# Kernel optimization log

Hardware: AMD Instinct MI355X
Metric: run time of the kernel (lower is better)

## Reference

```python
import jax, jax.numpy as jnp
import numpy as np

DIM = 1024
HEADS = 16
HEAD_DIM = DIM // HEADS
EPS = 1e-5


def setup_inputs() -> dict:
    key = jax.random.key(0)
    ks = jax.random.split(key, 4)
    N, L = 4, 2048
    x = jax.random.normal(ks[0], (N, L, DIM), dtype=jnp.float32)
    # causal mask: True means masked (strictly upper triangle)
    attn_mask = jnp.triu(jnp.ones((L, L), dtype=jnp.bool_), k=1)[None, None, :, :]
    w_qkv = jax.random.normal(ks[1], (3 * DIM, DIM), dtype=jnp.float32) * (DIM ** -0.5)
    w_proj = jax.random.normal(ks[2], (DIM, DIM), dtype=jnp.float32) * (DIM ** -0.5)
    b_proj = jnp.zeros((DIM,), dtype=jnp.float32)
    q_gamma = jnp.ones((HEAD_DIM,), dtype=jnp.float32)
    q_beta = jnp.zeros((HEAD_DIM,), dtype=jnp.float32)
    k_gamma = jnp.ones((HEAD_DIM,), dtype=jnp.float32)
    k_beta = jnp.zeros((HEAD_DIM,), dtype=jnp.float32)
    return {"x": x, "attn_mask": attn_mask, "w_qkv": w_qkv, "w_proj": w_proj,
            "b_proj": b_proj, "q_gamma": q_gamma, "q_beta": q_beta,
            "k_gamma": k_gamma, "k_beta": k_beta}


def _layernorm(h, gamma, beta):
    mu = jnp.mean(h, axis=-1, keepdims=True)
    var = jnp.mean(jnp.square(h - mu), axis=-1, keepdims=True)
    return (h - mu) * jax.lax.rsqrt(var + EPS) * gamma + beta


def reference(x, attn_mask, w_qkv, w_proj, b_proj, q_gamma, q_beta, k_gamma, k_beta):
    N, L, D = x.shape
    H, hd = HEADS, HEAD_DIM
    scale = hd ** -0.5
    qkv = jnp.einsum('nld,ed->nle', x, w_qkv)  # [N, L, 3D]
    qkv = qkv.reshape(N, L, 3, H, hd).transpose(2, 0, 3, 1, 4)  # [3, N, H, L, hd]
    q, k, v = qkv[0], qkv[1], qkv[2]
    q = _layernorm(q, q_gamma, q_beta)
    k = _layernorm(k, k_gamma, k_beta)
    scores = jnp.einsum('nhqd,nhkd->nhqk', q * scale, k)
    scores = scores + jnp.where(attn_mask, -jnp.inf, 0.0).astype(scores.dtype)
    attn = jax.nn.softmax(scores, axis=-1)
    out = jnp.einsum('nhqk,nhkd->nhqd', attn, v)  # [N, H, L, hd]
    out = out.transpose(0, 2, 1, 3).reshape(N, L, D)
    return jnp.einsum('nld,ed->nle', out, w_proj) + b_proj
```

## Files before the change

kernel.cpp:

```cpp
#include <hip/hip_runtime.h>


using f16x8 = __attribute__((ext_vector_type(8))) _Float16;
using f16x4 = __attribute__((ext_vector_type(4))) _Float16;
using f16x2 = __attribute__((ext_vector_type(2))) _Float16;
using f32x4 = __attribute__((ext_vector_type(4))) float;
using f32x16 = __attribute__((ext_vector_type(16))) float;
using u32x4 = __attribute__((ext_vector_type(4))) unsigned int;

#define MFMA16(a, b, c) __builtin_amdgcn_mfma_f32_16x16x32_f16(a, b, c, 0, 0, 0)
#define MFMA32(a, b, c) __builtin_amdgcn_mfma_f32_32x32x16_f16(a, b, c, 0, 0, 0)

__device__ __forceinline__ void gload_lds16(const void* g, void* l) {
  __builtin_amdgcn_global_load_lds(
      (const __attribute__((address_space(1))) unsigned int*)g,
      (__attribute__((address_space(3))) unsigned int*)l, 16, 0, 0);
}

__device__ __forceinline__ float dot2acc(unsigned int pk, float c) {
#if __has_builtin(__builtin_amdgcn_fdot2)
  const f16x2 ones = {(_Float16)1.f, (_Float16)1.f};
  return __builtin_amdgcn_fdot2(__builtin_bit_cast(f16x2, pk), ones, c, false);
#else
  f16x2 v = __builtin_bit_cast(f16x2, pk);
  return c + (float)v[0] + (float)v[1];
#endif
}

__global__ __launch_bounds__(256) void f32_to_f16_kernel(
    const float* __restrict__ in, _Float16* __restrict__ out, int n) {
  int i = (blockIdx.x * 256 + threadIdx.x) * 8;
  if (i >= n) return;
  float4 a = *(const float4*)(in + i);
  float4 b = *(const float4*)(in + i + 4);
  f16x8 o;
  o[0] = (_Float16)a.x; o[1] = (_Float16)a.y; o[2] = (_Float16)a.z; o[3] = (_Float16)a.w;
  o[4] = (_Float16)b.x; o[5] = (_Float16)b.y; o[6] = (_Float16)b.z; o[7] = (_Float16)b.w;
  *(f16x8*)(out + i) = o;
}

template <int MODE>
__global__ __launch_bounds__(256, 2) void gemm_bt(
    const _Float16* __restrict__ A, const _Float16* __restrict__ B,
    void* __restrict__ Cout, const float* __restrict__ bias,
    const float* __restrict__ qg, const float* __restrict__ qb,
    const float* __restrict__ kg, const float* __restrict__ kb,
    int M, int N, int K) {
  __shared__ __align__(16) _Float16 As[3][128 * 32];
  __shared__ __align__(16) _Float16 Bs[3][256 * 32];
  const int tid = threadIdx.x;
  const int w = tid >> 6, lane = tid & 63;
  const int c = lane & 15, g = lane >> 4;
  const long mbase = (long)blockIdx.x * 128;
  const long nbase = (long)blockIdx.y * 256;
  const int wm = (w >> 1) * 64, wn = (w & 1) * 128;
  const int sr4 = lane >> 2;
  const int scol = ((lane & 3) ^ ((lane >> 3) & 3)) * 8;
  const int sg = (g ^ ((c >> 1) & 3)) * 8;
  const char* pAr = (const char*)As + (wm + c) * 64 + sg * 2;
  const char* pBr = (const char*)Bs + (wn + c) * 64 + sg * 2;

#define GSTAGE(aOff_, bOff_, kt_)                                             \
  {                                                                           \
    const int kk_ = (kt_) * 32;                                               \
    _Pragma("unroll") for (int i = 0; i < 2; ++i) {                           \
      const int arow = w * 32 + i * 16 + sr4;                                 \
      gload_lds16(A + (mbase + arow) * K + kk_ + scol,                        \
                  (char*)As + (aOff_) + (w * 2 + i) * 1024);                  \
    }                                                                         \
    _Pragma("unroll") for (int j = 0; j < 4; ++j) {                           \
      const int brow = w * 64 + j * 16 + sr4;                                 \
      gload_lds16(B + (nbase + brow) * K + kk_ + scol,                        \
                  (char*)Bs + (bOff_) + (w * 4 + j) * 1024);                  \
    }                                                                         \
  }

  f32x4 acc[4][8];
#pragma unroll
  for (int i = 0; i < 4; ++i)
#pragma unroll
    for (int j = 0; j < 8; ++j) acc[i][j] = f32x4{0.f, 0.f, 0.f, 0.f};

  const int nk = K >> 5;
  GSTAGE(0, 0, 0);
  GSTAGE(8192, 16384, 1);
  int aR = 0, bR = 0;
  int aS = 16384, bS = 32768;
  for (int kt = 0; kt < nk; ++kt) {
    if (kt + 1 < nk) {
      asm volatile("s_waitcnt vmcnt(6)" ::: "memory");
    } else {
      asm volatile("s_waitcnt vmcnt(0)" ::: "memory");
    }
    __builtin_amdgcn_sched_barrier(0);
    __builtin_amdgcn_s_barrier();
    __builtin_amdgcn_sched_barrier(0);
    f16x8 af[4], bfr[8];
#pragma unroll
    for (int mt = 0; mt < 4; ++mt)
      af[mt] = *(const f16x8*)(pAr + aR + mt * 1024);
#pragma unroll
    for (int nt = 0; nt < 8; ++nt)
      bfr[nt] = *(const f16x8*)(pBr + bR + nt * 1024);
    if (kt + 2 < nk) GSTAGE(aS, bS, kt + 2);
    __builtin_amdgcn_s_setprio(1);
#pragma unroll
    for (int mt = 0; mt < 4; ++mt)
#pragma unroll
      for (int nt = 0; nt < 8; ++nt)
        acc[mt][nt] = MFMA16(af[mt], bfr[nt], acc[mt][nt]);
    __builtin_amdgcn_s_setprio(0);
    aR = (aR == 16384) ? 0 : aR + 8192;
    bR = (bR == 32768) ? 0 : bR + 16384;
    aS = (aS == 16384) ? 0 : aS + 8192;
    bS = (bS == 32768) ? 0 : bS + 16384;
  }
#undef GSTAGE

  if constexpr (MODE == 1) {
    const int region = (int)(nbase >> 10);
    if (region < 2) {
      const float* gamma = region ? kg : qg;
      const float* beta = region ? kb : qb;
      float gam[4], bet[4];
#pragma unroll
      for (int j = 0; j < 4; ++j) {
        gam[j] = gamma[j * 16 + c];
        bet[j] = beta[j * 16 + c];
      }
      const float sc = region ? 1.f : 0.1803368801111204f;
#pragma unroll
      for (int mt = 0; mt < 4; ++mt)
#pragma unroll
        for (int hh = 0; hh < 2; ++hh)
#pragma unroll
          for (int r = 0; r < 4; ++r) {
            float s1 = 0.f, s2 = 0.f;
#pragma unroll
            for (int j = 0; j < 4; ++j) {
              const float v = acc[mt][hh * 4 + j][r];
              s1 += v;
              s2 += v * v;
            }
#pragma unroll
            for (int msk = 1; msk < 16; msk <<= 1) {
              s1 += __shfl_xor(s1, msk);
              s2 += __shfl_xor(s2, msk);
            }
            const float mu = s1 * 0.015625f;
            const float rstd = rsqrtf(s2 * 0.015625f - mu * mu + 1e-5f);
#pragma unroll
            for (int j = 0; j < 4; ++j)
              acc[mt][hh * 4 + j][r] =
                  ((acc[mt][hh * 4 + j][r] - mu) * rstd * gam[j] + bet[j]) * sc;
          }
    }
#pragma unroll
    for (int nt = 0; nt < 8; ++nt) {
      const long col = nbase + wn + nt * 16 + c;
#pragma unroll
      for (int mt = 0; mt < 4; ++mt)
#pragma unroll
        for (int r = 0; r < 4; ++r) {
          const long row = mbase + wm + mt * 16 + g * 4 + r;
          ((_Float16*)Cout)[row * N + col] = (_Float16)acc[mt][nt][r];
        }
    }
  } else {
#pragma unroll
    for (int nt = 0; nt < 8; ++nt) {
      const long col = nbase + wn + nt * 16 + c;
      const float bv = bias ? bias[col] : 0.f;
#pragma unroll
      for (int mt = 0; mt < 4; ++mt)
#pragma unroll
        for (int r = 0; r < 4; ++r) {
          const long row = mbase + wm + mt * 16 + g * 4 + r;
          ((float*)Cout)[row * N + col] = acc[mt][nt][r] + bv;
        }
    }
  }
}

__global__ __launch_bounds__(256) void transpose_v_kernel(
    const _Float16* __restrict__ qkv, _Float16* __restrict__ Vt) {
  __shared__ __align__(16) _Float16 tile[64][80];
  const int nh = blockIdx.y;
  const long n = nh >> 4;
  const int h = nh & 15;
  const long lbase = (long)blockIdx.x * 64;
  const int t = threadIdx.x;
#pragma unroll
  for (int r = 0; r < 2; ++r) {
    const int l = (t + r * 256) >> 3;
    const int cc = (t & 7) * 8;
    f16x8 v = *(const f16x8*)(qkv + (n * 2048 + lbase + l) * 3072 + 2048 + h * 64 + cc);
    *(f16x8*)&tile[l][cc] = v;
  }
  __syncthreads();
  const int d = t >> 2, q = t & 3;
  f16x8 o0, o1;
#pragma unroll
  for (int i = 0; i < 8; ++i) {
    o0[i] = tile[q * 16 + i][d];
    o1[i] = tile[q * 16 + 8 + i][d];
  }
  _Float16* dst = Vt + ((long)nh * 64 + d) * 2048 + lbase + q * 16;
  *(f16x8*)dst = o0;
  *(f16x8*)(dst + 8) = o1;
}

__global__ __launch_bounds__(256, 4) void attn_kernel(
    const _Float16* __restrict__ qkv, const _Float16* __restrict__ Vt,
    _Float16* __restrict__ Ob) {
  __shared__ __align__(16) char lds[32768];
  const int w = threadIdx.x >> 6;
  const int lane = threadIdx.x & 63;
  const int c5 = lane & 31;
  const int hi = lane >> 5;
  const int nh = blockIdx.x;
  const long n = nh >> 4;
  const int h = nh & 15;
  const int qtile = 15 - blockIdx.y;
  const int qlo_blk = qtile * 128;
  const int qlo = qlo_blk + w * 32;
  const int qrow = qlo + c5;

  const _Float16* Qp = qkv + n * 2048 * 3072 + h * 64;
  const _Float16* Kq = Qp + 1024;
  const _Float16* Vp = Vt + (long)nh * 64 * 2048;

  const int sr8 = lane >> 3;
  const int scol = ((lane & 7) ^ sr8) * 8;

  const int nkv_blk = (qlo_blk + 191) >> 6;
  const int nkv_w = (qlo + 95) >> 6;

#define STAGE(BUF, kv_)                                                        \
  {                                                                            \
    const int kb_ = (kv_) * 64;                                                \
    _Pragma("unroll") for (int i = 0; i < 2; ++i) {                            \
      const int idx = w * 2 + i;                                               \
      const int row = idx * 8 + sr8;                                           \
      gload_lds16(Kq + (long)(kb_ + row) * 3072 + scol,                        \
                  lds + (BUF) * 8192 + idx * 1024);                            \
      gload_lds16(Vp + (long)row * 2048 + kb_ + scol,                          \
                  lds + 16384 + (BUF) * 8192 + idx * 1024);                    \
    }                                                                          \
  }

  f16x8 qf[4];
#pragma unroll
  for (int dc = 0; dc < 4; ++dc)
    qf[dc] = *(const f16x8*)(Qp + (long)qrow * 3072 + dc * 16 + hi * 8);

  f32x16 negM;
#pragma unroll
  for (int r = 0; r < 16; ++r) negM[r] = -12.0f;

  f32x16 acc[2];
#pragma unroll
  for (int db = 0; db < 2; ++db)
#pragma unroll
    for (int r = 0; r < 16; ++r) acc[db][r] = 0.f;
  float ls = 0.f;

  const int swr = c5 & 7;
  const char* Lb[4];
#pragma unroll
  for (int j = 0; j < 4; ++j)
    Lb[j] = lds + c5 * 128 + (((j * 2 + hi) ^ swr) << 4);

#define COMPUTE(BUF, kv_)                                                      \
  {                                                                            \
    const int kbase = (kv_) * 64;                                              \
    f32x16 s0, s1;                                                             \
    __builtin_amdgcn_s_setprio(1);                                             \
    {                                                                          \
      f16x8 kf0 = *(const f16x8*)(Lb[0] + (BUF) * 8192);                       \
      f16x8 kf1 = *(const f16x8*)(Lb[0] + (BUF) * 8192 + 4096);                \
      s0 = MFMA32(kf0, qf[0], negM);                                           \
      s1 = MFMA32(kf1, qf[0], negM);                                           \
    }                                                                          \
    _Pragma("unroll") for (int dc = 1; dc < 4; ++dc) {                         \
      f16x8 kf0 = *(const f16x8*)(Lb[dc] + (BUF) * 8192);                      \
      f16x8 kf1 = *(const f16x8*)(Lb[dc] + (BUF) * 8192 + 4096);               \
      s0 = MFMA32(kf0, qf[dc], s0);                                            \
      s1 = MFMA32(kf1, qf[dc], s1);                                            \
    }                                                                          \
    __builtin_amdgcn_s_setprio(0);                                             \
    if (kbase + 63 > qlo) {                                                    \
      _Pragma("unroll") for (int r = 0; r < 16; ++r) {                         \
        const int mv = (r & 3) + 8 * (r >> 2) + 4 * hi;                        \
        if (kbase + mv > qrow) s0[r] = -1e30f;                                 \
        if (kbase + 32 + mv > qrow) s1[r] = -1e30f;                            \
      }                                                                        \
    }                                                                          \
    _Pragma("unroll") for (int r = 0; r < 16; ++r) {                           \
      s0[r] = exp2f(s0[r]);                                                    \
      s1[r] = exp2f(s1[r]);                                                    \
    }                                                                          \
    unsigned int pk0[4][2], pk1[4][2];                                         \
    _Pragma("unroll") for (int r2 = 0; r2 < 4; ++r2)                           \
        _Pragma("unroll") for (int p = 0; p < 2; ++p) {                        \
      pk0[r2][p] = __builtin_bit_cast(                                         \
          unsigned int, __builtin_amdgcn_cvt_pkrtz(s0[4 * r2 + 2 * p],         \
                                                   s0[4 * r2 + 2 * p + 1]));   \
      pk1[r2][p] = __builtin_bit_cast(                                         \
          unsigned int, __builtin_amdgcn_cvt_pkrtz(s1[4 * r2 + 2 * p],         \
                                                   s1[4 * r2 + 2 * p + 1]));   \
    }                                                                          \
    _Pragma("unroll") for (int r2 = 0; r2 < 4; ++r2)                           \
        _Pragma("unroll") for (int p = 0; p < 2; ++p) {                        \
      ls = dot2acc(pk0[r2][p], ls);                                            \
      ls = dot2acc(pk1[r2][p], ls);                                            \
    }                                                                          \
    f16x8 pB[4];                                                               \
    _Pragma("unroll") for (int kk = 0; kk < 4; ++kk) {                         \
      const int rx = (kk & 1) * 2;                                             \
      unsigned int x0 = (kk < 2) ? pk0[rx][0] : pk1[rx][0];                    \
      unsigned int y0 = (kk < 2) ? pk0[rx + 1][0] : pk1[rx + 1][0];            \
      unsigned int x1 = (kk < 2) ? pk0[rx][1] : pk1[rx][1];                    \
      unsigned int y1 = (kk < 2) ? pk0[rx + 1][1] : pk1[rx + 1][1];            \
      asm("v_permlane32_swap_b32 %0, %1" : "+v"(x0), "+v"(y0));                \
      asm("v_permlane32_swap_b32 %0, %1" : "+v"(x1), "+v"(y1));                \
      pB[kk] = __builtin_bit_cast(f16x8, u32x4{x0, x1, y0, y1});               \
    }                                                                          \
    __builtin_amdgcn_s_setprio(1);                                             \
    _Pragma("unroll") for (int db = 0; db < 2; ++db)                           \
        _Pragma("unroll") for (int kk = 0; kk < 4; ++kk) {                     \
      f16x8 vf = *(const f16x8*)(Lb[kk] + 16384 + (BUF) * 8192 + db * 4096);   \
      acc[db] = MFMA32(vf, pB[kk], acc[db]);                                   \
    }                                                                          \
    __builtin_amdgcn_s_setprio(0);                                             \
  }

  STAGE(0, 0);
  for (int kv = 0; kv < nkv_blk; kv += 2) {
    __syncthreads();
    if (kv + 1 < nkv_blk) STAGE(1, kv + 1);
    if (kv < nkv_w) COMPUTE(0, kv);
    if (kv + 1 >= nkv_blk) break;
    __syncthreads();
    if (kv + 2 < nkv_blk) STAGE(0, kv + 2);
    if (kv + 1 < nkv_w) COMPUTE(1, kv + 1);
  }
#undef COMPUTE
#undef STAGE

  const float lsr = ls + __shfl_xor(ls, 32);
  const float inv = 1.f / lsr;
  _Float16* ob = Ob + ((long)(n * 2048) + qrow) * 1024 + h * 64 + 4 * hi;
#pragma unroll
  for (int db = 0; db < 2; ++db)
#pragma unroll
    for (int r2 = 0; r2 < 4; ++r2) {
      f16x4 o;
#pragma unroll
      for (int j = 0; j < 4; ++j)
        o[j] = (_Float16)(acc[db][4 * r2 + j] * inv);
      *(f16x4*)(ob + db * 32 + 8 * r2) = o;
    }
}

extern "C" void kernel_launch(void* const* d_in, const int* in_sizes, int n_in,
                              void* d_out, int out_size, void* d_ws, size_t ws_size,
                              hipStream_t stream) {
  const float* x = (const float*)d_in[0];
  const float* w_qkv = (const float*)d_in[2];
  const float* w_proj = (const float*)d_in[3];
  const float* b_proj = (const float*)d_in[4];
  const float* qg = (const float*)d_in[5];
  const float* qb = (const float*)d_in[6];
  const float* kg = (const float*)d_in[7];
  const float* kb = (const float*)d_in[8];

  char* ws = (char*)d_ws;
  _Float16* xb     = (_Float16*)(ws + 0);
  _Float16* wqkvb  = (_Float16*)(ws + 16777216);
  _Float16* wprojb = (_Float16*)(ws + 23068672);
  _Float16* qkvh   = (_Float16*)(ws + 25165824);
  _Float16* Vt     = (_Float16*)(ws + 75497472);
  _Float16* Ob     = xb;

  f32_to_f16_kernel<<<4096, 256, 0, stream>>>(x, xb, 8388608);
  f32_to_f16_kernel<<<1536, 256, 0, stream>>>(w_qkv, wqkvb, 3145728);
  f32_to_f16_kernel<<<512, 256, 0, stream>>>(w_proj, wprojb, 1048576);

  gemm_bt<1><<<dim3(64, 12), 256, 0, stream>>>(xb, wqkvb, qkvh, nullptr,
                                               qg, qb, kg, kb, 8192, 3072, 1024);
  transpose_v_kernel<<<dim3(32, 64), 256, 0, stream>>>(qkvh, Vt);
  attn_kernel<<<dim3(64, 16), 256, 0, stream>>>(qkvh, Vt, Ob);
  gemm_bt<0><<<dim3(64, 4), 256, 0, stream>>>(Ob, wprojb, d_out, b_proj,
                                              nullptr, nullptr, nullptr, nullptr,
                                              8192, 1024, 1024);
}
```

Baseline: 195.1 us.

## Fuse V transpose into QKV GEMM epilogue and merge fp32-to-fp16 conversions

Blocks of the QKV GEMM that cover the V region now stage their tile in shared memory, transposed, and write V directly in the [n,h,d,L] layout. This removes the separate transpose kernel along with its extra read and write of V. The V part of qkvh is no longer written, so attention must read V only from Vt. The three conversion launches are also merged into one kernel that selects its source by index, which saves launch overhead.

```diff
diff --git a/kernel.cpp b/kernel.cpp
--- a/kernel.cpp
+++ b/kernel.cpp
@@ -27,27 +27,37 @@
 #endif
 }
 
-__global__ __launch_bounds__(256) void f32_to_f16_kernel(
-    const float* __restrict__ in, _Float16* __restrict__ out, int n) {
-  int i = (blockIdx.x * 256 + threadIdx.x) * 8;
-  if (i >= n) return;
-  float4 a = *(const float4*)(in + i);
-  float4 b = *(const float4*)(in + i + 4);
+__global__ __launch_bounds__(256) void convert_all_kernel(
+    const float* __restrict__ x, const float* __restrict__ wq,
+    const float* __restrict__ wp, _Float16* __restrict__ xb,
+    _Float16* __restrict__ wqb, _Float16* __restrict__ wpb) {
+  long i = ((long)blockIdx.x * 256 + threadIdx.x) * 8;
+  const float* src;
+  _Float16* dst;
+  if (i < 8388608) {
+    src = x; dst = xb;
+  } else if (i < 8388608 + 3145728) {
+    src = wq + (i - 8388608); dst = wqb + (i - 8388608); i = 0;
+  } else {
+    src = wp + (i - 11534336); dst = wpb + (i - 11534336); i = 0;
+  }
+  float4 a = *(const float4*)(src + i);
+  float4 b = *(const float4*)(src + i + 4);
   f16x8 o;
   o[0] = (_Float16)a.x; o[1] = (_Float16)a.y; o[2] = (_Float16)a.z; o[3] = (_Float16)a.w;
   o[4] = (_Float16)b.x; o[5] = (_Float16)b.y; o[6] = (_Float16)b.z; o[7] = (_Float16)b.w;
-  *(f16x8*)(out + i) = o;
+  *(f16x8*)(dst + i) = o;
 }
 
 template <int MODE>
 __global__ __launch_bounds__(256, 2) void gemm_bt(
     const _Float16* __restrict__ A, const _Float16* __restrict__ B,
-    void* __restrict__ Cout, const float* __restrict__ bias,
+    void* __restrict__ Cout, _Float16* __restrict__ Vt,
+    const float* __restrict__ bias,
     const float* __restrict__ qg, const float* __restrict__ qb,
     const float* __restrict__ kg, const float* __restrict__ kb,
     int M, int N, int K) {
-  __shared__ __align__(16) _Float16 As[3][128 * 32];
-  __shared__ __align__(16) _Float16 Bs[3][256 * 32];
+  __shared__ __align__(16) char smem[73728];
   const int tid = threadIdx.x;
   const int w = tid >> 6, lane = tid & 63;
   const int c = lane & 15, g = lane >> 4;
@@ -57,8 +67,8 @@
   const int sr4 = lane >> 2;
   const int scol = ((lane & 3) ^ ((lane >> 3) & 3)) * 8;
   const int sg = (g ^ ((c >> 1) & 3)) * 8;
-  const char* pAr = (const char*)As + (wm + c) * 64 + sg * 2;
-  const char* pBr = (const char*)Bs + (wn + c) * 64 + sg * 2;
+  const char* pAr = smem + (wm + c) * 64 + sg * 2;
+  const char* pBr = smem + 24576 + (wn + c) * 64 + sg * 2;
 
 #define GSTAGE(aOff_, bOff_, kt_)                                             \
   {                                                                           \
@@ -66,12 +76,12 @@
     _Pragma("unroll") for (int i = 0; i < 2; ++i) {                           \
       const int arow = w * 32 + i * 16 + sr4;                                 \
       gload_lds16(A + (mbase + arow) * K + kk_ + scol,                        \
-                  (char*)As + (aOff_) + (w * 2 + i) * 1024);                  \
+                  smem + (aOff_) + (w * 2 + i) * 1024);                       \
     }                                                                         \
     _Pragma("unroll") for (int j = 0; j < 4; ++j) {                           \
       const int brow = w * 64 + j * 16 + sr4;                                 \
       gload_lds16(B + (nbase + brow) * K + kk_ + scol,                        \
-                  (char*)Bs + (bOff_) + (w * 4 + j) * 1024);                  \
+                  smem + 24576 + (bOff_) + (w * 4 + j) * 1024);               \
     }                                                                         \
   }
 
@@ -119,42 +129,65 @@
 
   if constexpr (MODE == 1) {
     const int region = (int)(nbase >> 10);
-    if (region < 2) {
-      const float* gamma = region ? kg : qg;
-      const float* beta = region ? kb : qb;
-      float gam[4], bet[4];
-#pragma unroll
-      for (int j = 0; j < 4; ++j) {
-        gam[j] = gamma[j * 16 + c];
-        bet[j] = beta[j * 16 + c];
+    if (region == 2) {
+      __syncthreads();
+      _Float16* T = (_Float16*)smem;
+#pragma unroll
+      for (int nt = 0; nt < 8; ++nt) {
+        const int dloc = wn + nt * 16 + c;
+#pragma unroll
+        for (int mt = 0; mt < 4; ++mt) {
+          const int lloc = wm + mt * 16 + g * 4;
+          f16x4 o;
+#pragma unroll
+          for (int r = 0; r < 4; ++r) o[r] = (_Float16)acc[mt][nt][r];
+          *(f16x4*)(T + dloc * 136 + lloc) = o;
+        }
       }
-      const float sc = region ? 1.f : 0.1803368801111204f;
-#pragma unroll
-      for (int mt = 0; mt < 4; ++mt)
-#pragma unroll
-        for (int hh = 0; hh < 2; ++hh)
-#pragma unroll
-          for (int r = 0; r < 4; ++r) {
-            float s1 = 0.f, s2 = 0.f;
-#pragma unroll
-            for (int j = 0; j < 4; ++j) {
-              const float v = acc[mt][hh * 4 + j][r];
-              s1 += v;
-              s2 += v * v;
-            }
-#pragma unroll
-            for (int msk = 1; msk < 16; msk <<= 1) {
-              s1 += __shfl_xor(s1, msk);
-              s2 += __shfl_xor(s2, msk);
-            }
-            const float mu = s1 * 0.015625f;
-            const float rstd = rsqrtf(s2 * 0.015625f - mu * mu + 1e-5f);
-#pragma unroll
-            for (int j = 0; j < 4; ++j)
-              acc[mt][hh * 4 + j][r] =
-                  ((acc[mt][hh * 4 + j][r] - mu) * rstd * gam[j] + bet[j]) * sc;
+      __syncthreads();
+      const long n = mbase >> 11;
+      const long lbase = mbase & 2047;
+      const long dcol = (nbase - 2048) + tid;
+      _Float16* dst = Vt + (n * 1024 + dcol) * 2048 + lbase;
+#pragma unroll
+      for (int j = 0; j < 16; ++j)
+        *(f16x8*)(dst + j * 8) = *(const f16x8*)(T + tid * 136 + j * 8);
+      return;
+    }
+    const float* gamma = region ? kg : qg;
+    const float* beta = region ? kb : qb;
+    float gam[4], bet[4];
+#pragma unroll
+    for (int j = 0; j < 4; ++j) {
+      gam[j] = gamma[j * 16 + c];
+      bet[j] = beta[j * 16 + c];
+    }
+    const float sc = region ? 1.f : 0.1803368801111204f;
+#pragma unroll
+    for (int mt = 0; mt < 4; ++mt)
+#pragma unroll
+      for (int hh = 0; hh < 2; ++hh)
+#pragma unroll
+        for (int r = 0; r < 4; ++r) {
+          float s1 = 0.f, s2 = 0.f;
+#pragma unroll
+          for (int j = 0; j < 4; ++j) {
+            const float v = acc[mt][hh * 4 + j][r];
+            s1 += v;
+            s2 += v * v;
           }
-    }
+#pragma unroll
+          for (int msk = 1; msk < 16; msk <<= 1) {
+            s1 += __shfl_xor(s1, msk);
+            s2 += __shfl_xor(s2, msk);
+          }
+          const float mu = s1 * 0.015625f;
+          const float rstd = rsqrtf(s2 * 0.015625f - mu * mu + 1e-5f);
+#pragma unroll
+          for (int j = 0; j < 4; ++j)
+            acc[mt][hh * 4 + j][r] =
+                ((acc[mt][hh * 4 + j][r] - mu) * rstd * gam[j] + bet[j]) * sc;
+        }
 #pragma unroll
     for (int nt = 0; nt < 8; ++nt) {
       const long col = nbase + wn + nt * 16 + c;
@@ -180,34 +213,6 @@
         }
     }
   }
-}
-
-__global__ __launch_bounds__(256) void transpose_v_kernel(
-    const _Float16* __restrict__ qkv, _Float16* __restrict__ Vt) {
-  __shared__ __align__(16) _Float16 tile[64][80];
-  const int nh = blockIdx.y;
-  const long n = nh >> 4;
-  const int h = nh & 15;
-  const long lbase = (long)blockIdx.x * 64;
-  const int t = threadIdx.x;
-#pragma unroll
-  for (int r = 0; r < 2; ++r) {
-    const int l = (t + r * 256) >> 3;
-    const int cc = (t & 7) * 8;
-    f16x8 v = *(const f16x8*)(qkv + (n * 2048 + lbase + l) * 3072 + 2048 + h * 64 + cc);
-    *(f16x8*)&tile[l][cc] = v;
-  }
-  __syncthreads();
-  const int d = t >> 2, q = t & 3;
-  f16x8 o0, o1;
-#pragma unroll
-  for (int i = 0; i < 8; ++i) {
-    o0[i] = tile[q * 16 + i][d];
-    o1[i] = tile[q * 16 + 8 + i][d];
-  }
-  _Float16* dst = Vt + ((long)nh * 64 + d) * 2048 + lbase + q * 16;
-  *(f16x8*)dst = o0;
-  *(f16x8*)(dst + 8) = o1;
 }
 
 __global__ __launch_bounds__(256, 4) void attn_kernel(
@@ -383,15 +388,13 @@
   _Float16* Vt     = (_Float16*)(ws + 75497472);
   _Float16* Ob     = xb;
 
-  f32_to_f16_kernel<<<4096, 256, 0, stream>>>(x, xb, 8388608);
-  f32_to_f16_kernel<<<1536, 256, 0, stream>>>(w_qkv, wqkvb, 3145728);
-  f32_to_f16_kernel<<<512, 256, 0, stream>>>(w_proj, wprojb, 1048576);
-
-  gemm_bt<1><<<dim3(64, 12), 256, 0, stream>>>(xb, wqkvb, qkvh, nullptr,
+  convert_all_kernel<<<6144, 256, 0, stream>>>(x, w_qkv, w_proj,
+                                               xb, wqkvb, wprojb);
+
+  gemm_bt<1><<<dim3(64, 12), 256, 0, stream>>>(xb, wqkvb, qkvh, Vt, nullptr,
                                                qg, qb, kg, kb, 8192, 3072, 1024);
-  transpose_v_kernel<<<dim3(32, 64), 256, 0, stream>>>(qkvh, Vt);
   attn_kernel<<<dim3(64, 16), 256, 0, stream>>>(qkvh, Vt, Ob);
-  gemm_bt<0><<<dim3(64, 4), 256, 0, stream>>>(Ob, wprojb, d_out, b_proj,
+  gemm_bt<0><<<dim3(64, 4), 256, 0, stream>>>(Ob, wprojb, d_out, nullptr, b_proj,
                                               nullptr, nullptr, nullptr, nullptr,
                                               8192, 1024, 1024);
 }
```

Result: no change. 192.9 us (-1.1%).
